# Kernel tuning notes

Hardware: AMD Instinct MI355X
Metric: run time of the kernel (lower is better)

The kernel has to match this reference:

```python
import jax, jax.numpy as jnp
import numpy as np

DIM = 1024
NUM_HEADS = 16
HEAD_DIM = DIM // NUM_HEADS


def setup_inputs() -> dict:
    key = jax.random.key(0)
    k_x, k_wqkv, k_bqkv, k_wo, k_bo = jax.random.split(key, 5)
    B, N = 2, 2048
    s = 1.0 / np.sqrt(DIM)
    return {
        "x": jax.random.normal(k_x, (B, N, DIM), dtype=jnp.float32),
        "w_qkv": jax.random.uniform(k_wqkv, (DIM, 3 * DIM), jnp.float32, -s, s),
        "b_qkv": jax.random.uniform(k_bqkv, (3 * DIM,), jnp.float32, -s, s),
        "w_out": jax.random.uniform(k_wo, (DIM, DIM), jnp.float32, -s, s),
        "b_out": jax.random.uniform(k_bo, (DIM,), jnp.float32, -s, s),
    }


def reference(x, w_qkv, b_qkv, w_out, b_out):
    B, N, D = x.shape
    H, Hd = NUM_HEADS, HEAD_DIM
    scale = Hd ** -0.5
    qkv = x @ w_qkv + b_qkv                      # [B,N,3D]
    qkv = qkv.reshape(B, N, 3, H, Hd).transpose(2, 0, 3, 1, 4)  # [3,B,H,N,Hd]
    q, k, v = qkv[0], qkv[1], qkv[2]
    scores = jnp.einsum("bhqd,bhkd->bhqk", q, k) * scale
    attn = jax.nn.softmax(scores, axis=-1)
    out = jnp.einsum("bhqk,bhkd->bhqd", attn, v)  # [B,H,N,Hd]
    out = out.transpose(0, 2, 1, 3).reshape(B, N, D)
    return out @ w_out + b_out
```

## Files before the change

### kernel.cpp

```cpp
#include <hip/hip_runtime.h>
#include <stdint.h>

#define D_MODEL 1024
#define NHEADS 16
#define HDIM 64
#define BATCH 2
#define SEQ 2048
#define MTOK (BATCH*SEQ)

typedef unsigned short u16;
typedef __attribute__((ext_vector_type(8))) __bf16 bf16x8;
typedef __attribute__((ext_vector_type(8))) unsigned short u16x8;
typedef __attribute__((ext_vector_type(4))) unsigned short u16x4;
typedef __attribute__((ext_vector_type(4))) float f32x4;
typedef __attribute__((ext_vector_type(16))) float f32x16;
typedef __attribute__((ext_vector_type(2))) unsigned int u32x2;

__device__ __forceinline__ u16 f2bf(float f) {
  union { float f; uint32_t u; } v; v.f = f;
  uint32_t u = v.u;
  u += 0x7fffu + ((u >> 16) & 1u);
  return (u16)(u >> 16);
}

__device__ __forceinline__ u16 f2bf_hw(float f) {
  return __builtin_bit_cast(u16, (__bf16)f);
}

__device__ __forceinline__ unsigned cvtpk(float a, float b) {
  unsigned r;
  asm("v_cvt_pk_bf16_f32 %0, %1, %2" : "=v"(r) : "v"(a), "v"(b));
  return r;
}

__device__ __forceinline__ u32x2 plswap(unsigned a, unsigned b) {
#if __has_builtin(__builtin_amdgcn_permlane32_swap)
  return __builtin_amdgcn_permlane32_swap(a, b, false, false);
#else
  asm("v_permlane32_swap_b32 %0, %1" : "+v"(a), "+v"(b));
  u32x2 r; r.x = a; r.y = b; return r;
#endif
}

__device__ __forceinline__ void async16(u16* lds, const u16* g) {
  __builtin_amdgcn_global_load_lds(
      (__attribute__((address_space(1))) void*)(u16*)g,
      (__attribute__((address_space(3))) void*)lds,
      16, 0, 0);
}

__device__ __forceinline__ void transpose_cast_body(
    const float* __restrict__ in, u16* __restrict__ out, int R, int C,
    int bid, int tid, float (*tile)[33])
{
  int nCB = C >> 5;
  int bc = bid % nCB, br = bid / nCB;
  int r0 = br * 32, c0 = bc * 32;
  int tx = tid & 31, ty = tid >> 5;
#pragma unroll
  for (int i = 0; i < 4; ++i)
    tile[ty + i*8][tx] = in[(size_t)(r0 + ty + i*8) * C + c0 + tx];
  __syncthreads();
#pragma unroll
  for (int i = 0; i < 4; ++i)
    out[(size_t)(c0 + ty + i*8) * R + r0 + tx] = f2bf(tile[tx][ty + i*8]);
}

__global__ __launch_bounds__(256) void prep_kernel(
    const float* __restrict__ x, const float* __restrict__ w_qkv,
    const float* __restrict__ w_out,
    u16* __restrict__ x_bf, u16* __restrict__ wqkv_t, u16* __restrict__ wout_t)
{
  __shared__ float tile[32][33];
  int bid = blockIdx.x, tid = threadIdx.x;
  if (bid < 2048) {
    int i = bid * 256 + tid;
    const float4* p = (const float4*)(x + (size_t)i * 8);
    float4 a = p[0], b = p[1];
    u16x8 r;
    r[0]=f2bf(a.x); r[1]=f2bf(a.y); r[2]=f2bf(a.z); r[3]=f2bf(a.w);
    r[4]=f2bf(b.x); r[5]=f2bf(b.y); r[6]=f2bf(b.z); r[7]=f2bf(b.w);
    *(u16x8*)(x_bf + (size_t)i * 8) = r;
  } else if (bid < 2048 + 3072) {
    transpose_cast_body(w_qkv, wqkv_t, 1024, 3072, bid - 2048, tid, tile);
  } else {
    transpose_cast_body(w_out, wout_t, 1024, 1024, bid - 5120, tid, tile);
  }
}

template <int EPI>
__global__ __launch_bounds__(512, 4) void gemm_bt_kernel(
    const u16* __restrict__ A, const u16* __restrict__ Bt,
    const float* __restrict__ bias,
    float* __restrict__ outF,
    u16* __restrict__ qb, u16* __restrict__ kb, u16* __restrict__ vt,
    int M, int Nn, int K)
{
  __shared__ alignas(16) u16 As[2][128 * 64];
  __shared__ alignas(16) u16 Bs[2][128 * 64];

  const int tid = threadIdx.x;
  const int wid = tid >> 6, lane = tid & 63;
  const int col = lane & 15, kg = lane >> 4;
  const int csw = (col & 7) << 3;

  const int nTN = Nn >> 7;
  int bidx = blockIdx.x;
  {
    int cpx = gridDim.x >> 3;
    bidx = (bidx & 7) * cpx + (bidx >> 3);
  }
  const int tile_m = (bidx / nTN) << 7;
  const int tile_n = (bidx % nTN) << 7;
  const int wm = (wid >> 2) << 6;
  const int wn = (wid & 3) << 5;

  f32x4 acc[4][2] = {};

  const int sr = tid >> 3;
  const int sc = (tid & 7) << 3;
  const int ssc = sc ^ ((sr & 7) << 3);

#define STAGE(buf, kt)                                                        \
  {                                                                           \
    _Pragma("unroll")                                                         \
    for (int i = 0; i < 2; ++i)                                               \
      async16(&As[buf][(i*64 + sr) * 64 + sc],                                \
              A + (size_t)(tile_m + i*64 + sr) * K + (kt)*64 + ssc);          \
    _Pragma("unroll")                                                         \
    for (int i = 0; i < 2; ++i)                                               \
      async16(&Bs[buf][(i*64 + sr) * 64 + sc],                                \
              Bt + (size_t)(tile_n + i*64 + sr) * K + (kt)*64 + ssc);         \
  }

  const int nk = K >> 6;
  STAGE(0, 0);
  __syncthreads();
  int cur = 0;

  for (int kt = 0; kt < nk; ++kt) {
    if (kt + 1 < nk) STAGE(cur ^ 1, kt + 1);

#pragma unroll
    for (int ks = 0; ks < 2; ++ks) {
      bf16x8 af[4], bfv[2];
#pragma unroll
      for (int i = 0; i < 4; ++i)
        af[i] = *(const bf16x8*)&As[cur][(wm + i*16 + col) * 64 + ((ks*32 + kg*8) ^ csw)];
#pragma unroll
      for (int j = 0; j < 2; ++j)
        bfv[j] = *(const bf16x8*)&Bs[cur][(wn + j*16 + col) * 64 + ((ks*32 + kg*8) ^ csw)];
#pragma unroll
      for (int i = 0; i < 4; ++i)
#pragma unroll
        for (int j = 0; j < 2; ++j)
          acc[i][j] = __builtin_amdgcn_mfma_f32_16x16x32_bf16(af[i], bfv[j], acc[i][j], 0, 0, 0);
    }

    __syncthreads();
    cur ^= 1;
  }
#undef STAGE

#pragma unroll
  for (int i = 0; i < 4; ++i) {
#pragma unroll
    for (int jn = 0; jn < 2; ++jn) {
      const int gcol = tile_n + wn + jn*16 + col;
      const float bv = bias[gcol];
      const int grow0 = tile_m + wm + i*16 + kg*4;
      if (EPI == 1) {
#pragma unroll
        for (int j = 0; j < 4; ++j)
          outF[(size_t)(grow0 + j) * Nn + gcol] = acc[i][jn][j] + bv;
      } else {
        const int btok = grow0 >> 11, tok0 = grow0 & 2047;
        const int which = gcol >> 10, f = gcol & 1023;
        const int h = f >> 6, hd = f & 63;
        if (which == 2) {
          u16x4 pk;
#pragma unroll
          for (int j = 0; j < 4; ++j) pk[j] = f2bf(acc[i][jn][j] + bv);
          *(u16x4*)&vt[((size_t)(btok*NHEADS + h) * HDIM + hd) * SEQ + tok0] = pk;
        } else {
#pragma unroll
          for (int j = 0; j < 4; ++j) {
            float val = acc[i][jn][j] + bv;
            size_t dst = ((size_t)(btok*NHEADS + h) * SEQ + tok0 + j) * HDIM + hd;
            if (which == 0) qb[dst] = f2bf(val * 0.18033688f);
            else            kb[dst] = f2bf(val);
          }
        }
      }
    }
  }
}

__global__ __launch_bounds__(256, 2) void attn_kernel(
    const u16* __restrict__ qb, const u16* __restrict__ kb,
    const u16* __restrict__ vt, u16* __restrict__ ao)
{
  __shared__ alignas(16) u16 Ks[128 * 64];
  __shared__ alignas(16) u16 Vs[64 * 128];

  const int tid = threadIdx.x, wid = tid >> 6, lane = tid & 63;
  const int c31 = lane & 31, hi = lane >> 5;
  const int rsw = (lane & 7) << 3;

  int bidx = blockIdx.x;
  bidx = (bidx & 7) * 64 + (bidx >> 3);
  const int bh = bidx >> 4;
  const int qt = bidx & 15;

  const u16* Qh = qb + (size_t)bh * SEQ * HDIM;
  const u16* Kh = kb + (size_t)bh * SEQ * HDIM;
  const u16* Vh = vt + (size_t)bh * SEQ * HDIM;

  const int q0 = qt * 128 + wid * 32;
  bf16x8 qf[4];
#pragma unroll
  for (int kk = 0; kk < 4; ++kk)
    qf[kk] = *(const bf16x8*)(Qh + (size_t)(q0 + c31) * HDIM + kk*16 + hi*8);

  float l_run = 0.f;
  f32x16 o[2] = {};

  const int krow = tid >> 1, kc = (tid & 1) << 5, ksw = (krow & 7) << 3;
  const int vrow = tid >> 2, vc = (tid & 3) << 5, vsw = (vrow & 7) << 3;

  u16x8 kreg[4], vreg[4];
#define LOAD_TILES(t)                                                               \
  {                                                                                 \
    _Pragma("unroll")                                                               \
    for (int i = 0; i < 4; ++i)                                                     \
      kreg[i] = *(const u16x8*)(Kh + (size_t)((t)*128 + krow) * HDIM + kc + i*8);   \
    _Pragma("unroll")                                                               \
    for (int i = 0; i < 4; ++i)                                                     \
      vreg[i] = *(const u16x8*)(Vh + (size_t)vrow * SEQ + (t)*128 + vc + i*8);      \
  }

  LOAD_TILES(0);

  for (int t = 0; t < 16; ++t) {
    __syncthreads();
#pragma unroll
    for (int i = 0; i < 4; ++i)
      *(u16x8*)&Ks[krow * 64 + ((kc + i*8) ^ ksw)] = kreg[i];
#pragma unroll
    for (int i = 0; i < 4; ++i)
      *(u16x8*)&Vs[vrow * 128 + ((vc + i*8) ^ vsw)] = vreg[i];
    __syncthreads();
    if (t < 15) LOAD_TILES(t + 1);

    f32x16 s[4] = {};
#pragma unroll
    for (int kk = 0; kk < 4; ++kk) {
#pragma unroll
      for (int nt = 0; nt < 4; ++nt) {
        bf16x8 kf = *(const bf16x8*)&Ks[(nt*32 + c31) * 64 + ((kk*16 + hi*8) ^ rsw)];
        s[nt] = __builtin_amdgcn_mfma_f32_32x32x16_bf16(kf, qf[kk], s[nt], 0, 0, 0);
      }
    }

#pragma unroll
    for (int nt = 0; nt < 4; ++nt) {
      float sum = 0.f;
#pragma unroll
      for (int r = 0; r < 16; ++r) {
        s[nt][r] = __builtin_amdgcn_exp2f(s[nt][r]);
        sum += s[nt][r];
      }
      l_run += sum;
    }

#pragma unroll
    for (int kk = 0; kk < 8; ++kk) {
      const int nt = kk >> 1, rb = (kk & 1) * 8;
      unsigned A0 = cvtpk(s[nt][rb+0], s[nt][rb+1]);
      unsigned A1 = cvtpk(s[nt][rb+2], s[nt][rb+3]);
      unsigned B0 = cvtpk(s[nt][rb+4], s[nt][rb+5]);
      unsigned B1 = cvtpk(s[nt][rb+6], s[nt][rb+7]);
      u32x2 p0 = plswap(A0, B0);
      u32x2 p1 = plswap(A1, B1);
      union { unsigned w[4]; bf16x8 v; } pf;
      pf.w[0] = p0.x; pf.w[1] = p1.x; pf.w[2] = p0.y; pf.w[3] = p1.y;
#pragma unroll
      for (int dt = 0; dt < 2; ++dt) {
        bf16x8 vf = *(const bf16x8*)&Vs[(dt*32 + c31) * 128 + ((kk*16 + hi*8) ^ rsw)];
        o[dt] = __builtin_amdgcn_mfma_f32_32x32x16_bf16(vf, pf.v, o[dt], 0, 0, 0);
      }
    }
  }

  const int bb = bh >> 4, h = bh & 15;
  {
    float l = l_run + __shfl_xor(l_run, 32);
    float inv = 1.0f / l;
    const int nrow = q0 + c31;
#pragma unroll
    for (int dt = 0; dt < 2; ++dt) {
#pragma unroll
      for (int tq = 0; tq < 4; ++tq) {
        u16x4 pk;
#pragma unroll
        for (int j = 0; j < 4; ++j) pk[j] = f2bf(o[dt][tq*4 + j] * inv);
        int feat = h*64 + dt*32 + tq*8 + hi*4;
        *(u16x4*)&ao[(size_t)(bb * SEQ + nrow) * D_MODEL + feat] = pk;
      }
    }
  }
#undef LOAD_TILES
}

extern "C" void kernel_launch(void* const* d_in, const int* in_sizes, int n_in,
                              void* d_out, int out_size, void* d_ws, size_t ws_size,
                              hipStream_t stream)
{
  const float* x     = (const float*)d_in[0];
  const float* w_qkv = (const float*)d_in[1];
  const float* b_qkv = (const float*)d_in[2];
  const float* w_out = (const float*)d_in[3];
  const float* b_out = (const float*)d_in[4];
  float* out = (float*)d_out;
  (void)in_sizes; (void)n_in; (void)out_size; (void)ws_size;

  char* ws = (char*)d_ws;
  u16* x_bf   = (u16*)(ws);
  u16* wqkv_t = (u16*)(ws + (size_t)( 8 << 20));
  u16* wout_t = (u16*)(ws + (size_t)(14 << 20));
  u16* qb     = (u16*)(ws + (size_t)(16 << 20));
  u16* kb     = (u16*)(ws + (size_t)(24 << 20));
  u16* vt     = (u16*)(ws + (size_t)(32 << 20));
  u16* ao     = (u16*)(ws + (size_t)(40 << 20));

  prep_kernel<<<2048 + 3072 + 1024, 256, 0, stream>>>(x, w_qkv, w_out, x_bf, wqkv_t, wout_t);

  gemm_bt_kernel<0><<<(MTOK/128)*(3072/128), 512, 0, stream>>>(
      x_bf, wqkv_t, b_qkv, nullptr, qb, kb, vt, MTOK, 3072, 1024);

  attn_kernel<<<32*16, 256, 0, stream>>>(qb, kb, vt, ao);

  gemm_bt_kernel<1><<<(MTOK/128)*(1024/128), 512, 0, stream>>>(
      ao, wout_t, b_out, out, nullptr, nullptr, nullptr, MTOK, 1024, 1024);
}
```

Baseline: 112.8 us.

## Single-buffer GEMM shared tiles to raise occupancy

Removes the double-buffered LDS staging in the bf16 GEMM and uses one A/B tile, loaded and synchronized each k-step. The launch bound's minimum blocks per CU goes from 4 to 6, so halved LDS and a tighter register budget should fit more resident blocks. In exchange the prefetch overlap of the next tile with MFMA compute is lost, and an extra barrier per iteration serializes load and compute within each block.

```diff
diff --git a/kernel.cpp b/kernel.cpp
--- a/kernel.cpp
+++ b/kernel.cpp
@@ -89,15 +89,15 @@
 }
 
 template <int EPI>
-__global__ __launch_bounds__(512, 4) void gemm_bt_kernel(
+__global__ __launch_bounds__(512, 6) void gemm_bt_kernel(
     const u16* __restrict__ A, const u16* __restrict__ Bt,
     const float* __restrict__ bias,
     float* __restrict__ outF,
     u16* __restrict__ qb, u16* __restrict__ kb, u16* __restrict__ vt,
     int M, int Nn, int K)
 {
-  __shared__ alignas(16) u16 As[2][128 * 64];
-  __shared__ alignas(16) u16 Bs[2][128 * 64];
+  __shared__ alignas(16) u16 As[128 * 64];
+  __shared__ alignas(16) u16 Bs[128 * 64];
 
   const int tid = threadIdx.x;
   const int wid = tid >> 6, lane = tid & 63;
@@ -121,46 +121,35 @@
   const int sc = (tid & 7) << 3;
   const int ssc = sc ^ ((sr & 7) << 3);
 
-#define STAGE(buf, kt)                                                        \
-  {                                                                           \
-    _Pragma("unroll")                                                         \
-    for (int i = 0; i < 2; ++i)                                               \
-      async16(&As[buf][(i*64 + sr) * 64 + sc],                                \
-              A + (size_t)(tile_m + i*64 + sr) * K + (kt)*64 + ssc);          \
-    _Pragma("unroll")                                                         \
-    for (int i = 0; i < 2; ++i)                                               \
-      async16(&Bs[buf][(i*64 + sr) * 64 + sc],                                \
-              Bt + (size_t)(tile_n + i*64 + sr) * K + (kt)*64 + ssc);         \
-  }
-
   const int nk = K >> 6;
-  STAGE(0, 0);
-  __syncthreads();
-  int cur = 0;
-
   for (int kt = 0; kt < nk; ++kt) {
-    if (kt + 1 < nk) STAGE(cur ^ 1, kt + 1);
+    __syncthreads();
+#pragma unroll
+    for (int i = 0; i < 2; ++i)
+      async16(&As[(i*64 + sr) * 64 + sc],
+              A + (size_t)(tile_m + i*64 + sr) * K + kt*64 + ssc);
+#pragma unroll
+    for (int i = 0; i < 2; ++i)
+      async16(&Bs[(i*64 + sr) * 64 + sc],
+              Bt + (size_t)(tile_n + i*64 + sr) * K + kt*64 + ssc);
+    __syncthreads();
 
 #pragma unroll
     for (int ks = 0; ks < 2; ++ks) {
       bf16x8 af[4], bfv[2];
 #pragma unroll
       for (int i = 0; i < 4; ++i)
-        af[i] = *(const bf16x8*)&As[cur][(wm + i*16 + col) * 64 + ((ks*32 + kg*8) ^ csw)];
+        af[i] = *(const bf16x8*)&As[(wm + i*16 + col) * 64 + ((ks*32 + kg*8) ^ csw)];
 #pragma unroll
       for (int j = 0; j < 2; ++j)
-        bfv[j] = *(const bf16x8*)&Bs[cur][(wn + j*16 + col) * 64 + ((ks*32 + kg*8) ^ csw)];
+        bfv[j] = *(const bf16x8*)&Bs[(wn + j*16 + col) * 64 + ((ks*32 + kg*8) ^ csw)];
 #pragma unroll
       for (int i = 0; i < 4; ++i)
 #pragma unroll
         for (int j = 0; j < 2; ++j)
           acc[i][j] = __builtin_amdgcn_mfma_f32_16x16x32_bf16(af[i], bfv[j], acc[i][j], 0, 0, 0);
     }
-
-    __syncthreads();
-    cur ^= 1;
-  }
-#undef STAGE
+  }
 
 #pragma unroll
   for (int i = 0; i < 4; ++i) {
```

Measured after the change: 109.7 us. 1.03x faster.
